# Optimization experiments

Measured on AMD Instinct MI355X. Metric: run time of the kernel, lower is better.

## Reference

```python
import jax, jax.numpy as jnp
import numpy as np

B, H = 1024, 256
HP = H // 2  # hyperparams_dim
W_SCALE = 0.08  # kaiming-uniform-like magnitude to keep tanh unsaturated


def setup_inputs() -> dict:
    key = jax.random.key(0)
    ks = jax.random.split(key, 8)
    return {
        "h_0": jax.random.normal(ks[0], (B, 1, H), dtype=jnp.float32),
        "h_t": jax.random.normal(ks[1], (B, 1, H), dtype=jnp.float32),
        "msg": jax.random.normal(ks[2], (B, 1, H), dtype=jnp.float32),
        "c": jax.random.uniform(ks[3], (1,), dtype=jnp.float32),
        "fc1_w": jax.random.normal(ks[4], (HP, H), dtype=jnp.float32) * W_SCALE,
        "fc2_w": jax.random.normal(ks[5], (HP, HP), dtype=jnp.float32) * W_SCALE,
        "fc3_w": jax.random.normal(ks[6], (HP, HP), dtype=jnp.float32) * W_SCALE,
        "fc4_w": jax.random.normal(ks[7], (2 * H * H, HP), dtype=jnp.float32) * W_SCALE,
    }


def reference(h_0, h_t, msg, c, fc1_w, fc2_w, fc3_w, fc4_w):
    # torch code clamps self.c into [0, 1] before use
    cc = jnp.clip(c, 0.0, 1.0)
    h = cc * h_0 + (1.0 - cc) * h_t                     # [B, 1, H]
    x = jnp.tanh(jnp.einsum('bsh,ph->bsp', h, fc1_w))    # [B, 1, HP]
    x = jnp.tanh(jnp.einsum('bsp,qp->bsq', x, fc2_w))    # [B, 1, HP]
    x = jnp.tanh(jnp.einsum('bsq,rq->bsr', x, fc3_w))    # [B, 1, HP]
    f4 = jnp.einsum('bsr,wr->bsw', x, fc4_w)             # [B, 1, 2*H*H]
    g1 = f4[..., : H * H].reshape(-1, H, H)              # [B, H, H]
    g2 = f4[..., H * H :].reshape(-1, H, H)              # [B, H, H]
    # F.linear(msg[i], g) == msg[i] @ g.T, batched over B
    g1_out = jnp.tanh(jnp.einsum('bsh,bkh->bsk', msg, g1))  # [B, 1, H]
    out = jnp.einsum('bsk,bok->bso', g1_out, g2)             # [B, 1, H]
    return out
```

## Files before the change

kernel.cpp:

```cpp
#include <hip/hip_runtime.h>
#include <hip/hip_bf16.h>

#define HDIM 256
#define HPDIM 128

typedef short bf8 __attribute__((ext_vector_type(8)));
typedef float f32x4 __attribute__((ext_vector_type(4)));

__device__ inline unsigned pkbf2(float a, float b) {
  float2 f; f.x = a; f.y = b;
  __hip_bfloat162 h = __float22bfloat162_rn(f);
  unsigned u; __builtin_memcpy(&u, &h, 4); return u;
}
__device__ inline unsigned short bfbits(float v) {
  __hip_bfloat16 h = __float2bfloat16(v);
  unsigned short u; __builtin_memcpy(&u, &h, 2); return u;
}
__device__ inline uint4 pack8u(float4 a, float4 b) {
  uint4 r;
  r.x = pkbf2(a.x, a.y); r.y = pkbf2(a.z, a.w);
  r.z = pkbf2(b.x, b.y); r.w = pkbf2(b.z, b.w);
  return r;
}
__device__ inline float fast_tanh(float x) {
  float t = __expf(2.0f * x);
  return 1.0f - 2.0f * __builtin_amdgcn_rcpf(t + 1.0f);
}

__global__ __launch_bounds__(256) void k_fmt(
    const float* __restrict__ w1, const float* __restrict__ w2,
    const float* __restrict__ w3, const float* __restrict__ msg,
    short* __restrict__ wf, float* __restrict__ msgTT) {
  __shared__ float T[64][257];
  const int t = threadIdx.x;
  if (blockIdx.x < 32) {
    int u = blockIdx.x * 256 + t;
    const float* src; short* dst; int row, c, Kt;
    if (u < 4096)      { src = w1; dst = wf;          Kt = 8; row = u >> 5; c = u & 31; }
    else if (u < 6144) { src = w2; dst = wf + 32768;  Kt = 4; row = (u-4096) >> 4; c = (u-4096) & 15; }
    else               { src = w3; dst = wf + 49152;  Kt = 4; row = (u-6144) >> 4; c = (u-6144) & 15; }
    int ks = c >> 2, q = c & 3, Kd = Kt * 32;
    const float* s = src + row * Kd + ks * 32 + q * 8;
    float4 a = *(const float4*)s, b = *(const float4*)(s + 4);
    int P = row >> 4, r16 = row & 15;
    int outl = ((P * Kt + ks) * 64 + q * 16 + r16);
    *(uint4*)(dst + (size_t)outl * 8) = pack8u(a, b);
  } else {
    const int b0 = (blockIdx.x - 32) * 64;
    #pragma unroll 4
    for (int it = 0; it < 16; ++it) {
      int flat = it * 1024 + t * 4;
      int row = flat >> 8, col = flat & 255;
      float4 v = *(const float4*)(msg + (b0 + row) * HDIM + col);
      T[row][col] = v.x; T[row][col+1] = v.y; T[row][col+2] = v.z; T[row][col+3] = v.w;
    }
    __syncthreads();
    const int bloc = t & 63;
    #pragma unroll 4
    for (int it = 0; it < 16; ++it) {
      int g = it * 4 + (t >> 6);
      float4 v; v.x = T[bloc][g*4]; v.y = T[bloc][g*4+1];
                v.z = T[bloc][g*4+2]; v.w = T[bloc][g*4+3];
      *(float4*)(msgTT + (size_t)g * 4096 + (b0 + bloc) * 4) = v;
    }
  }
}

__global__ __launch_bounds__(256) void k_mlp(
    const float* __restrict__ h0, const float* __restrict__ htv,
    const float* __restrict__ cp, const short* __restrict__ wf,
    short* __restrict__ x3f) {
  __shared__ char hbuf[8192];
  __shared__ char xa[4096];
  __shared__ char xb[4096];
  const int t = threadIdx.x, wave = t >> 6, lane = t & 63;
  const int r16 = lane & 15, quad = lane >> 4;
  const int b0 = blockIdx.x * 16;
  const float cc = fminf(fmaxf(cp[0], 0.f), 1.f);

  #pragma unroll
  for (int it = 0; it < 2; ++it) {
    int flat = it * 2048 + t * 8;
    int row = flat >> 8, col = flat & 255, kb = col >> 3;
    int gi = (b0 + row) * HDIM + col;
    float4 a = *(const float4*)(h0 + gi);
    float4 b = *(const float4*)(htv + gi);
    float4 va, vb;
    va.x = cc*a.x + (1.f-cc)*b.x; va.y = cc*a.y + (1.f-cc)*b.y;
    va.z = cc*a.z + (1.f-cc)*b.z; va.w = cc*a.w + (1.f-cc)*b.w;
    a = *(const float4*)(h0 + gi + 4); b = *(const float4*)(htv + gi + 4);
    vb.x = cc*a.x + (1.f-cc)*b.x; vb.y = cc*a.y + (1.f-cc)*b.y;
    vb.z = cc*a.z + (1.f-cc)*b.z; vb.w = cc*a.w + (1.f-cc)*b.w;
    *(uint4*)(hbuf + row*512 + ((kb ^ (row & 7)) << 4)) = pack8u(va, vb);
  }
  __syncthreads();

  {
    f32x4 acc[2] = {};
    #pragma unroll
    for (int ks = 0; ks < 8; ++ks) {
      bf8 af = *(bf8*)(hbuf + r16*512 + (((ks*4 + quad) ^ (r16 & 7)) << 4));
      #pragma unroll
      for (int nt = 0; nt < 2; ++nt) {
        bf8 bw_ = *(const bf8*)(wf + (size_t)(((wave*2 + nt)*8 + ks)*64 + lane)*8);
        acc[nt] = __builtin_amdgcn_mfma_f32_16x16x32_bf16(af, bw_, acc[nt], 0, 0, 0);
      }
    }
    #pragma unroll
    for (int nt = 0; nt < 2; ++nt)
      #pragma unroll
      for (int i = 0; i < 4; ++i) {
        int row = quad*4 + i, col = wave*32 + nt*16 + r16;
        *(unsigned short*)(xa + row*256 + (((col >> 3) ^ (row & 7)) << 4) + ((col & 7) << 1))
            = bfbits(fast_tanh(acc[nt][i]));
      }
  }
  __syncthreads();
  {
    f32x4 acc[2] = {};
    #pragma unroll
    for (int ks = 0; ks < 4; ++ks) {
      bf8 af = *(bf8*)(xa + r16*256 + (((ks*4 + quad) ^ (r16 & 7)) << 4));
      #pragma unroll
      for (int nt = 0; nt < 2; ++nt) {
        bf8 bw_ = *(const bf8*)(wf + 32768 + (size_t)(((wave*2 + nt)*4 + ks)*64 + lane)*8);
        acc[nt] = __builtin_amdgcn_mfma_f32_16x16x32_bf16(af, bw_, acc[nt], 0, 0, 0);
      }
    }
    #pragma unroll
    for (int nt = 0; nt < 2; ++nt)
      #pragma unroll
      for (int i = 0; i < 4; ++i) {
        int row = quad*4 + i, col = wave*32 + nt*16 + r16;
        *(unsigned short*)(xb + row*256 + (((col >> 3) ^ (row & 7)) << 4) + ((col & 7) << 1))
            = bfbits(fast_tanh(acc[nt][i]));
      }
  }
  __syncthreads();
  {
    f32x4 acc[2] = {};
    #pragma unroll
    for (int ks = 0; ks < 4; ++ks) {
      bf8 af = *(bf8*)(xb + r16*256 + (((ks*4 + quad) ^ (r16 & 7)) << 4));
      #pragma unroll
      for (int nt = 0; nt < 2; ++nt) {
        bf8 bw_ = *(const bf8*)(wf + 49152 + (size_t)(((wave*2 + nt)*4 + ks)*64 + lane)*8);
        acc[nt] = __builtin_amdgcn_mfma_f32_16x16x32_bf16(af, bw_, acc[nt], 0, 0, 0);
      }
    }
    #pragma unroll
    for (int nt = 0; nt < 2; ++nt)
      #pragma unroll
      for (int i = 0; i < 4; ++i) {
        int row = quad*4 + i, col = wave*32 + nt*16 + r16;
        *(unsigned short*)(xa + row*256 + (((col >> 3) ^ (row & 7)) << 4) + ((col & 7) << 1))
            = bfbits(fast_tanh(acc[nt][i]));
      }
  }
  __syncthreads();
  {
    int ks = t >> 6, l = t & 63, q2 = l >> 4, rr = l & 15;
    uint4 d = *(uint4*)(xa + rr*256 + (((ks*4 + q2) ^ (rr & 7)) << 4));
    *(uint4*)(x3f + (size_t)((blockIdx.x*4 + ks)*64 + l)*8) = d;
  }
}

template<int PHASE>
__global__ __launch_bounds__(256, 4) void k_hyper(
    const short* __restrict__ x3f, const float* __restrict__ wTT,
    const float* __restrict__ fc4, float* __restrict__ outp) {
  __shared__ char lds[32768];
  const int kcol = blockIdx.x;
  const int t = threadIdx.x, wave = t >> 6, lane = t & 63;
  const int r16 = lane & 15, quad = lane >> 4;
  const int bw = blockIdx.y * 256 + wave * 64;

  bf8 xf[4][4];
  #pragma unroll
  for (int nt = 0; nt < 4; ++nt)
    #pragma unroll
    for (int ks = 0; ks < 4; ++ks)
      xf[nt][ks] = *(const bf8*)(x3f +
          (size_t)(((blockIdx.y*16 + wave*4 + nt)*4 + ks)*64 + lane)*8);

  const float* src = fc4 + ((size_t)(PHASE ? 65536 : 0) + (size_t)kcol * 256) * HPDIM;
  float gacc[4] = {0.f, 0.f, 0.f, 0.f};

  #pragma unroll 1
  for (int half = 0; half < 2; ++half) {
    #pragma unroll
    for (int it = 0; it < 8; ++it) {
      int flat = it * 2048 + t * 8;
      int row = flat >> 7, kb = t & 15;
      float4 a = *(const float4*)(src + half*16384 + flat);
      float4 b = *(const float4*)(src + half*16384 + flat + 4);
      *(uint4*)(lds + row*256 + ((kb ^ (row & 7)) << 4)) = pack8u(a, b);
    }
    __syncthreads();

    #pragma unroll 2
    for (int ht = 0; ht < 8; ++ht) {
      const int hb = half*32 + ht*4 + quad;
      float4 wv[4];
      #pragma unroll
      for (int nt = 0; nt < 4; ++nt)
        wv[nt] = *(const float4*)(wTT + (size_t)hb*4096 + (bw + nt*16 + r16)*4);
      const int row = ht*16 + r16;
      bf8 af[4];
      #pragma unroll
      for (int ks = 0; ks < 4; ++ks)
        af[ks] = *(bf8*)(lds + row*256 + (((ks*4 + quad) ^ (row & 7)) << 4));
      #pragma unroll
      for (int nt = 0; nt < 4; ++nt) {
        f32x4 acc = {};
        #pragma unroll
        for (int ks = 0; ks < 4; ++ks)
          acc = __builtin_amdgcn_mfma_f32_16x16x32_bf16(af[ks], xf[nt][ks], acc, 0, 0, 0);
        gacc[nt] += acc[0]*wv[nt].x + acc[1]*wv[nt].y + acc[2]*wv[nt].z + acc[3]*wv[nt].w;
      }
    }
    __syncthreads();
  }

  #pragma unroll
  for (int nt = 0; nt < 4; ++nt) {
    float v = gacc[nt];
    v += __shfl_xor(v, 16);
    v += __shfl_xor(v, 32);
    if (quad == 0) {
      int b = bw + nt*16 + r16;
      if (PHASE == 0) outp[(size_t)(kcol >> 2)*4096 + b*4 + (kcol & 3)] = fast_tanh(v);
      else            outp[b*HDIM + kcol] = v;
    }
  }
}

extern "C" void kernel_launch(void* const* d_in, const int* in_sizes, int n_in,
                              void* d_out, int out_size, void* d_ws, size_t ws_size,
                              hipStream_t stream) {
  const float* h0  = (const float*)d_in[0];
  const float* htt = (const float*)d_in[1];
  const float* msg = (const float*)d_in[2];
  const float* c   = (const float*)d_in[3];
  const float* w1  = (const float*)d_in[4];
  const float* w2  = (const float*)d_in[5];
  const float* w3  = (const float*)d_in[6];
  const float* w4  = (const float*)d_in[7];
  float* out = (float*)d_out;

  short* x3f  = (short*)d_ws;
  float* g1TT = (float*)((char*)d_ws + 262144);
  float* msgTT= (float*)((char*)d_ws + 262144 + 1048576);
  short* wf   = (short*)((char*)d_ws + 262144 + 2097152);

  k_fmt<<<dim3(48), dim3(256), 0, stream>>>(w1, w2, w3, msg, wf, msgTT);
  k_mlp<<<dim3(64), dim3(256), 0, stream>>>(h0, htt, c, wf, x3f);
  k_hyper<0><<<dim3(256, 4), dim3(256), 0, stream>>>(x3f, msgTT, w4, g1TT);
  k_hyper<1><<<dim3(256, 4), dim3(256), 0, stream>>>(x3f, g1TT, w4, out);
}
```

Measured before the change: 181.8 us.

## Double-buffer fc4 tiles in LDS and process two output columns per block

Each k_hyper block now handles two fc4 output columns instead of one, so every wTT vector it loads is reused for twice as many MFMA results. The fc4 weights are staged through a double-buffered 64KB LDS region, with the register prefetch of the next chunk overlapping the MFMA compute on the current one. This aims to hide global load latency and cut redundant wTT traffic. In exchange the grid is halved, LDS use per block doubles, and launch bounds drop to 2 blocks per CU, which lowers occupancy and adds register pressure from the prefetch buffers.

```diff
diff --git a/kernel.cpp b/kernel.cpp
--- a/kernel.cpp
+++ b/kernel.cpp
@@ -166,11 +166,11 @@
 }
 
 template<int PHASE>
-__global__ __launch_bounds__(256, 4) void k_hyper(
+__global__ __launch_bounds__(256, 2) void k_hyper(
     const short* __restrict__ x3f, const float* __restrict__ wTT,
     const float* __restrict__ fc4, float* __restrict__ outp) {
-  __shared__ char lds[32768];
-  const int kcol = blockIdx.x;
+  __shared__ char lds[65536];
+  const int kp = blockIdx.x;
   const int t = threadIdx.x, wave = t >> 6, lane = t & 63;
   const int r16 = lane & 15, quad = lane >> 4;
   const int bw = blockIdx.y * 256 + wave * 64;
@@ -183,56 +183,79 @@
       xf[nt][ks] = *(const bf8*)(x3f +
           (size_t)(((blockIdx.y*16 + wave*4 + nt)*4 + ks)*64 + lane)*8);
 
-  const float* src = fc4 + ((size_t)(PHASE ? 65536 : 0) + (size_t)kcol * 256) * HPDIM;
-  float gacc[4] = {0.f, 0.f, 0.f, 0.f};
-
-  #pragma unroll 1
-  for (int half = 0; half < 2; ++half) {
-    #pragma unroll
-    for (int it = 0; it < 8; ++it) {
-      int flat = it * 2048 + t * 8;
-      int row = flat >> 7, kb = t & 15;
-      float4 a = *(const float4*)(src + half*16384 + flat);
-      float4 b = *(const float4*)(src + half*16384 + flat + 4);
-      *(uint4*)(lds + row*256 + ((kb ^ (row & 7)) << 4)) = pack8u(a, b);
-    }
-    __syncthreads();
-
-    #pragma unroll 2
-    for (int ht = 0; ht < 8; ++ht) {
-      const int hb = half*32 + ht*4 + quad;
+  const float* src0 = fc4 + ((size_t)(PHASE ? 65536 : 0) + (size_t)kp * 512) * HPDIM;
+  const int srow = t >> 2, scol = (t & 3) * 32;
+  float4 ra[2][8];
+  float gacc[2][4] = {};
+
+  auto LD = [&](int r) {
+    #pragma unroll
+    for (int kc = 0; kc < 2; ++kc) {
+      const float* s = src0 + ((size_t)(kc*256 + r*64 + srow))*HPDIM + scol;
+      #pragma unroll
+      for (int j = 0; j < 8; ++j) ra[kc][j] = *(const float4*)(s + 4*j);
+    }
+  };
+  auto ST = [&](int buf) {
+    #pragma unroll
+    for (int kc = 0; kc < 2; ++kc) {
+      char* base = lds + (buf*2 + kc)*16384 + srow*256;
+      #pragma unroll
+      for (int i = 0; i < 4; ++i) {
+        int kb = (t & 3)*4 + i;
+        *(uint4*)(base + ((kb ^ (srow & 7)) << 4)) = pack8u(ra[kc][2*i], ra[kc][2*i+1]);
+      }
+    }
+  };
+  auto COMP = [&](int r, int buf) {
+    #pragma unroll
+    for (int htl = 0; htl < 4; ++htl) {
+      const int row = htl*16 + r16;
+      const int hb = r*16 + htl*4 + quad;
       float4 wv[4];
       #pragma unroll
       for (int nt = 0; nt < 4; ++nt)
         wv[nt] = *(const float4*)(wTT + (size_t)hb*4096 + (bw + nt*16 + r16)*4);
-      const int row = ht*16 + r16;
-      bf8 af[4];
-      #pragma unroll
-      for (int ks = 0; ks < 4; ++ks)
-        af[ks] = *(bf8*)(lds + row*256 + (((ks*4 + quad) ^ (row & 7)) << 4));
-      #pragma unroll
-      for (int nt = 0; nt < 4; ++nt) {
-        f32x4 acc = {};
+      bf8 af[2][4];
+      #pragma unroll
+      for (int kc = 0; kc < 2; ++kc)
         #pragma unroll
         for (int ks = 0; ks < 4; ++ks)
-          acc = __builtin_amdgcn_mfma_f32_16x16x32_bf16(af[ks], xf[nt][ks], acc, 0, 0, 0);
-        gacc[nt] += acc[0]*wv[nt].x + acc[1]*wv[nt].y + acc[2]*wv[nt].z + acc[3]*wv[nt].w;
-      }
-    }
-    __syncthreads();
-  }
+          af[kc][ks] = *(bf8*)(lds + (buf*2 + kc)*16384 + row*256 +
+                               (((ks*4 + quad) ^ (row & 7)) << 4));
+      #pragma unroll
+      for (int kc = 0; kc < 2; ++kc)
+        #pragma unroll
+        for (int nt = 0; nt < 4; ++nt) {
+          f32x4 acc = {};
+          #pragma unroll
+          for (int ks = 0; ks < 4; ++ks)
+            acc = __builtin_amdgcn_mfma_f32_16x16x32_bf16(af[kc][ks], xf[nt][ks], acc, 0, 0, 0);
+          gacc[kc][nt] += acc[0]*wv[nt].x + acc[1]*wv[nt].y + acc[2]*wv[nt].z + acc[3]*wv[nt].w;
+        }
+    }
+  };
+
+  LD(0); ST(0); __syncthreads();
+  LD(1); COMP(0, 0); ST(1); __syncthreads();
+  LD(2); COMP(1, 1); ST(0); __syncthreads();
+  LD(3); COMP(2, 0); ST(1); __syncthreads();
+  COMP(3, 1);
 
   #pragma unroll
-  for (int nt = 0; nt < 4; ++nt) {
-    float v = gacc[nt];
-    v += __shfl_xor(v, 16);
-    v += __shfl_xor(v, 32);
-    if (quad == 0) {
-      int b = bw + nt*16 + r16;
-      if (PHASE == 0) outp[(size_t)(kcol >> 2)*4096 + b*4 + (kcol & 3)] = fast_tanh(v);
-      else            outp[b*HDIM + kcol] = v;
-    }
-  }
+  for (int kc = 0; kc < 2; ++kc)
+    #pragma unroll
+    for (int nt = 0; nt < 4; ++nt) {
+      float v = gacc[kc][nt];
+      v += __shfl_xor(v, 16);
+      v += __shfl_xor(v, 32);
+      if (quad == 0) {
+        int b = bw + nt*16 + r16;
+        int kcol = kp*2 + kc;
+        if (PHASE == 0) outp[(size_t)(kcol >> 2)*4096 + b*4 + (kcol & 3)] = fast_tanh(v);
+        else            outp[b*HDIM + kcol] = v;
+      }
+    }
 }
 
 extern "C" void kernel_launch(void* const* d_in, const int* in_sizes, int n_in,
@@ -255,6 +278,6 @@
 
   k_fmt<<<dim3(48), dim3(256), 0, stream>>>(w1, w2, w3, msg, wf, msgTT);
   k_mlp<<<dim3(64), dim3(256), 0, stream>>>(h0, htt, c, wf, x3f);
-  k_hyper<0><<<dim3(256, 4), dim3(256), 0, stream>>>(x3f, msgTT, w4, g1TT);
-  k_hyper<1><<<dim3(256, 4), dim3(256), 0, stream>>>(x3f, g1TT, w4, out);
-}
+  k_hyper<0><<<dim3(128, 4), dim3(256), 0, stream>>>(x3f, msgTT, w4, g1TT);
+  k_hyper<1><<<dim3(128, 4), dim3(256), 0, stream>>>(x3f, g1TT, w4, out);
+}
```

Result: slower. 424.4 us (+133.5%).

## Fuse weight formatting into MLP kernel, widen hyper blocks, prefetch wTT

Applied to the files above, without the earlier changes.

Merges the weight-format kernel and the MLP kernel into one launch: the MLP now reads fp32 fc1-3 weights directly and packs them to bf16 in registers, and the msg transpose runs in extra blocks of the same grid. The hyper kernels move to 512-thread blocks covering 512 batch rows, so each fc4 tile staged into LDS is reused by twice as many waves and the grid has half as many blocks. The per-iteration wTT loads are double-buffered one step ahead to hide latency. In exchange, the fused pre-kernel reserves about 66KB of shared memory per block, and the wider hyper blocks have lower occupancy and more register pressure.

```diff
diff --git a/kernel.cpp b/kernel.cpp
--- a/kernel.cpp
+++ b/kernel.cpp
@@ -22,58 +22,49 @@
   r.z = pkbf2(b.x, b.y); r.w = pkbf2(b.z, b.w);
   return r;
 }
+__device__ inline bf8 pack8v(float4 a, float4 b) {
+  union { bf8 v; uint4 u; } r; r.u = pack8u(a, b); return r.v;
+}
 __device__ inline float fast_tanh(float x) {
   float t = __expf(2.0f * x);
   return 1.0f - 2.0f * __builtin_amdgcn_rcpf(t + 1.0f);
 }
 
-__global__ __launch_bounds__(256) void k_fmt(
+__global__ __launch_bounds__(256) void k_pre(
+    const float* __restrict__ h0, const float* __restrict__ htv,
+    const float* __restrict__ cp, const float* __restrict__ msg,
     const float* __restrict__ w1, const float* __restrict__ w2,
-    const float* __restrict__ w3, const float* __restrict__ msg,
-    short* __restrict__ wf, float* __restrict__ msgTT) {
-  __shared__ float T[64][257];
-  const int t = threadIdx.x;
-  if (blockIdx.x < 32) {
-    int u = blockIdx.x * 256 + t;
-    const float* src; short* dst; int row, c, Kt;
-    if (u < 4096)      { src = w1; dst = wf;          Kt = 8; row = u >> 5; c = u & 31; }
-    else if (u < 6144) { src = w2; dst = wf + 32768;  Kt = 4; row = (u-4096) >> 4; c = (u-4096) & 15; }
-    else               { src = w3; dst = wf + 49152;  Kt = 4; row = (u-6144) >> 4; c = (u-6144) & 15; }
-    int ks = c >> 2, q = c & 3, Kd = Kt * 32;
-    const float* s = src + row * Kd + ks * 32 + q * 8;
-    float4 a = *(const float4*)s, b = *(const float4*)(s + 4);
-    int P = row >> 4, r16 = row & 15;
-    int outl = ((P * Kt + ks) * 64 + q * 16 + r16);
-    *(uint4*)(dst + (size_t)outl * 8) = pack8u(a, b);
-  } else {
-    const int b0 = (blockIdx.x - 32) * 64;
+    const float* __restrict__ w3,
+    short* __restrict__ x3f, float* __restrict__ msgTT) {
+  __shared__ char lds[66048];
+  const int t = threadIdx.x, wave = t >> 6, lane = t & 63;
+
+  if (blockIdx.x >= 64) {
+    float* T = (float*)lds;
+    const int b0 = (blockIdx.x - 64) * 64;
     #pragma unroll 4
     for (int it = 0; it < 16; ++it) {
       int flat = it * 1024 + t * 4;
       int row = flat >> 8, col = flat & 255;
       float4 v = *(const float4*)(msg + (b0 + row) * HDIM + col);
-      T[row][col] = v.x; T[row][col+1] = v.y; T[row][col+2] = v.z; T[row][col+3] = v.w;
+      T[row*257 + col]   = v.x; T[row*257 + col+1] = v.y;
+      T[row*257 + col+2] = v.z; T[row*257 + col+3] = v.w;
     }
     __syncthreads();
     const int bloc = t & 63;
     #pragma unroll 4
     for (int it = 0; it < 16; ++it) {
       int g = it * 4 + (t >> 6);
-      float4 v; v.x = T[bloc][g*4]; v.y = T[bloc][g*4+1];
-                v.z = T[bloc][g*4+2]; v.w = T[bloc][g*4+3];
+      float4 v; v.x = T[bloc*257 + g*4];   v.y = T[bloc*257 + g*4+1];
+                v.z = T[bloc*257 + g*4+2]; v.w = T[bloc*257 + g*4+3];
       *(float4*)(msgTT + (size_t)g * 4096 + (b0 + bloc) * 4) = v;
     }
-  }
-}
-
-__global__ __launch_bounds__(256) void k_mlp(
-    const float* __restrict__ h0, const float* __restrict__ htv,
-    const float* __restrict__ cp, const short* __restrict__ wf,
-    short* __restrict__ x3f) {
-  __shared__ char hbuf[8192];
-  __shared__ char xa[4096];
-  __shared__ char xb[4096];
-  const int t = threadIdx.x, wave = t >> 6, lane = t & 63;
+    return;
+  }
+
+  char* hbuf = lds;
+  char* xa   = lds + 8192;
+  char* xb   = lds + 12288;
   const int r16 = lane & 15, quad = lane >> 4;
   const int b0 = blockIdx.x * 16;
   const float cc = fminf(fmaxf(cp[0], 0.f), 1.f);
@@ -102,7 +93,8 @@
       bf8 af = *(bf8*)(hbuf + r16*512 + (((ks*4 + quad) ^ (r16 & 7)) << 4));
       #pragma unroll
       for (int nt = 0; nt < 2; ++nt) {
-        bf8 bw_ = *(const bf8*)(wf + (size_t)(((wave*2 + nt)*8 + ks)*64 + lane)*8);
+        const float* wp = w1 + ((wave*2 + nt)*16 + r16)*HDIM + ks*32 + quad*8;
+        bf8 bw_ = pack8v(*(const float4*)wp, *(const float4*)(wp + 4));
         acc[nt] = __builtin_amdgcn_mfma_f32_16x16x32_bf16(af, bw_, acc[nt], 0, 0, 0);
       }
     }
@@ -123,7 +115,8 @@
       bf8 af = *(bf8*)(xa + r16*256 + (((ks*4 + quad) ^ (r16 & 7)) << 4));
       #pragma unroll
       for (int nt = 0; nt < 2; ++nt) {
-        bf8 bw_ = *(const bf8*)(wf + 32768 + (size_t)(((wave*2 + nt)*4 + ks)*64 + lane)*8);
+        const float* wp = w2 + ((wave*2 + nt)*16 + r16)*HPDIM + ks*32 + quad*8;
+        bf8 bw_ = pack8v(*(const float4*)wp, *(const float4*)(wp + 4));
         acc[nt] = __builtin_amdgcn_mfma_f32_16x16x32_bf16(af, bw_, acc[nt], 0, 0, 0);
       }
     }
@@ -144,7 +137,8 @@
       bf8 af = *(bf8*)(xb + r16*256 + (((ks*4 + quad) ^ (r16 & 7)) << 4));
       #pragma unroll
       for (int nt = 0; nt < 2; ++nt) {
-        bf8 bw_ = *(const bf8*)(wf + 49152 + (size_t)(((wave*2 + nt)*4 + ks)*64 + lane)*8);
+        const float* wp = w3 + ((wave*2 + nt)*16 + r16)*HPDIM + ks*32 + quad*8;
+        bf8 bw_ = pack8v(*(const float4*)wp, *(const float4*)(wp + 4));
         acc[nt] = __builtin_amdgcn_mfma_f32_16x16x32_bf16(af, bw_, acc[nt], 0, 0, 0);
       }
     }
@@ -166,14 +160,14 @@
 }
 
 template<int PHASE>
-__global__ __launch_bounds__(256, 4) void k_hyper(
+__global__ __launch_bounds__(512, 2) void k_hyper(
     const short* __restrict__ x3f, const float* __restrict__ wTT,
     const float* __restrict__ fc4, float* __restrict__ outp) {
   __shared__ char lds[32768];
   const int kcol = blockIdx.x;
   const int t = threadIdx.x, wave = t >> 6, lane = t & 63;
   const int r16 = lane & 15, quad = lane >> 4;
-  const int bw = blockIdx.y * 256 + wave * 64;
+  const int bw = blockIdx.y * 512 + wave * 64;
 
   bf8 xf[4][4];
   #pragma unroll
@@ -181,16 +175,17 @@
     #pragma unroll
     for (int ks = 0; ks < 4; ++ks)
       xf[nt][ks] = *(const bf8*)(x3f +
-          (size_t)(((blockIdx.y*16 + wave*4 + nt)*4 + ks)*64 + lane)*8);
+          (size_t)(((blockIdx.y*32 + wave*4 + nt)*4 + ks)*64 + lane)*8);
 
   const float* src = fc4 + ((size_t)(PHASE ? 65536 : 0) + (size_t)kcol * 256) * HPDIM;
   float gacc[4] = {0.f, 0.f, 0.f, 0.f};
+  float4 wv[2][4];
 
   #pragma unroll 1
   for (int half = 0; half < 2; ++half) {
     #pragma unroll
-    for (int it = 0; it < 8; ++it) {
-      int flat = it * 2048 + t * 8;
+    for (int it = 0; it < 4; ++it) {
+      int flat = it * 4096 + t * 8;
       int row = flat >> 7, kb = t & 15;
       float4 a = *(const float4*)(src + half*16384 + flat);
       float4 b = *(const float4*)(src + half*16384 + flat + 4);
@@ -198,13 +193,20 @@
     }
     __syncthreads();
 
+    {
+      const int hb = half*32 + quad;
+      #pragma unroll
+      for (int nt = 0; nt < 4; ++nt)
+        wv[0][nt] = *(const float4*)(wTT + (size_t)hb*4096 + (bw + nt*16 + r16)*4);
+    }
     #pragma unroll 2
     for (int ht = 0; ht < 8; ++ht) {
-      const int hb = half*32 + ht*4 + quad;
-      float4 wv[4];
-      #pragma unroll
-      for (int nt = 0; nt < 4; ++nt)
-        wv[nt] = *(const float4*)(wTT + (size_t)hb*4096 + (bw + nt*16 + r16)*4);
+      if (ht < 7) {
+        const int hb = half*32 + (ht+1)*4 + quad;
+        #pragma unroll
+        for (int nt = 0; nt < 4; ++nt)
+          wv[(ht+1)&1][nt] = *(const float4*)(wTT + (size_t)hb*4096 + (bw + nt*16 + r16)*4);
+      }
       const int row = ht*16 + r16;
       bf8 af[4];
       #pragma unroll
@@ -216,7 +218,8 @@
         #pragma unroll
         for (int ks = 0; ks < 4; ++ks)
           acc = __builtin_amdgcn_mfma_f32_16x16x32_bf16(af[ks], xf[nt][ks], acc, 0, 0, 0);
-        gacc[nt] += acc[0]*wv[nt].x + acc[1]*wv[nt].y + acc[2]*wv[nt].z + acc[3]*wv[nt].w;
+        float4 w = wv[ht&1][nt];
+        gacc[nt] += acc[0]*w.x + acc[1]*w.y + acc[2]*w.z + acc[3]*w.w;
       }
     }
     __syncthreads();
@@ -251,10 +254,8 @@
   short* x3f  = (short*)d_ws;
   float* g1TT = (float*)((char*)d_ws + 262144);
   float* msgTT= (float*)((char*)d_ws + 262144 + 1048576);
-  short* wf   = (short*)((char*)d_ws + 262144 + 2097152);
-
-  k_fmt<<<dim3(48), dim3(256), 0, stream>>>(w1, w2, w3, msg, wf, msgTT);
-  k_mlp<<<dim3(64), dim3(256), 0, stream>>>(h0, htt, c, wf, x3f);
-  k_hyper<0><<<dim3(256, 4), dim3(256), 0, stream>>>(x3f, msgTT, w4, g1TT);
-  k_hyper<1><<<dim3(256, 4), dim3(256), 0, stream>>>(x3f, g1TT, w4, out);
-}
+
+  k_pre<<<dim3(80), dim3(256), 0, stream>>>(h0, htt, c, msg, w1, w2, w3, x3f, msgTT);
+  k_hyper<0><<<dim3(256, 2), dim3(512), 0, stream>>>(x3f, msgTT, w4, g1TT);
+  k_hyper<1><<<dim3(256, 2), dim3(512), 0, stream>>>(x3f, g1TT, w4, out);
+}
```

Result: slower. 282.9 us (+55.6%).
